# Kernel tuning notes

Hardware: AMD Instinct MI355X
Metric: run time of the kernel (lower is better)

Reference implementation:

```python
import jax, jax.numpy as jnp
import numpy as np
import math

B, T, H, D = 4, 2048, 16, 64
C = H * D            # d_model = 1024
FF = 4096            # mlp_hidden_dim
N_LAYERS = 12
EPS = 1e-5


def setup_inputs() -> dict:
    key = jax.random.key(0)
    ks = jax.random.split(key, 8)
    res_scale = 1.0 / math.sqrt(2 * N_LAYERS)
    std_c = math.sqrt(2.0 / C)
    std_ff = math.sqrt(2.0 / FF)
    return {
        "x": jax.random.normal(ks[0], (B, T, C), jnp.float32),
        "ln1_w": jnp.ones((C,), jnp.float32),
        "ln1_b": jnp.zeros((C,), jnp.float32),
        # weights stored [in, out] (transposed vs torch nn.Linear.weight)
        "w_qkv": jax.random.normal(ks[1], (C, 3 * C), jnp.float32) * std_c,
        "b_qkv": jnp.zeros((3 * C,), jnp.float32),
        "w_o": jax.random.normal(ks[2], (C, C), jnp.float32) * std_c * res_scale,
        "b_o": jnp.zeros((C,), jnp.float32),
        "ln2_w": jnp.ones((C,), jnp.float32),
        "ln2_b": jnp.zeros((C,), jnp.float32),
        "w_fc": jax.random.normal(ks[3], (C, FF), jnp.float32) * std_c,
        "b_fc": jnp.zeros((FF,), jnp.float32),
        "w_out": jax.random.normal(ks[4], (FF, C), jnp.float32) * std_ff * res_scale,
        "b_out": jnp.zeros((C,), jnp.float32),
    }


def _layer_norm(x, w, b):
    m = jnp.mean(x, axis=-1, keepdims=True)
    v = jnp.mean(jnp.square(x - m), axis=-1, keepdims=True)
    return (x - m) * jax.lax.rsqrt(v + EPS) * w + b


def reference(x, ln1_w, ln1_b, w_qkv, b_qkv, w_o, b_o, ln2_w, ln2_b, w_fc, b_fc, w_out, b_out):
    Bx, Tx, Cx = x.shape
    # attention
    qkv = _layer_norm(x, ln1_w, ln1_b) @ w_qkv + b_qkv          # [B,T,3C]
    q, k, v = jnp.split(qkv, 3, axis=-1)
    q = q.reshape(Bx, Tx, H, D)
    k = k.reshape(Bx, Tx, H, D)
    v = v.reshape(Bx, Tx, H, D)
    att = jnp.einsum("bqhd,bkhd->bhqk", q, k) / math.sqrt(D)    # [B,H,T,T]
    mask = jnp.tril(jnp.ones((Tx, Tx), dtype=bool))
    att = jnp.where(mask, att, -jnp.inf)
    att = jax.nn.softmax(att, axis=-1)
    y = jnp.einsum("bhqk,bkhd->bqhd", att, v).reshape(Bx, Tx, Cx)
    x = x + y @ w_o + b_o
    # mlp (torch F.gelu default = exact erf gelu)
    h = jax.nn.gelu(_layer_norm(x, ln2_w, ln2_b) @ w_fc + b_fc, approximate=False)
    x = x + h @ w_out + b_out
    return x
```

## Files before the change

### kernel.cpp

```cpp
#include <hip/hip_runtime.h>
#include <hip/hip_bf16.h>
#include <cstdint>


#define B_ 4
#define T_ 2048
#define H_ 16
#define D_ 64
#define C_ 1024
#define FF_ 4096
#define M_ (B_ * T_)
#define QKV_N (3 * C_)

typedef __bf16 bf16x8 __attribute__((ext_vector_type(8)));
typedef __bf16 bf16x4 __attribute__((ext_vector_type(4)));
typedef float floatx4 __attribute__((ext_vector_type(4)));

#define MFMA16(a, b, c) __builtin_amdgcn_mfma_f32_16x16x32_bf16(a, b, c, 0, 0, 0)

__device__ __forceinline__ void gload16(const void* g, void* l) {
  __builtin_amdgcn_global_load_lds(
      (const __attribute__((address_space(1))) void*)g,
      (__attribute__((address_space(3))) void*)l, 16, 0, 0);
}

__device__ __forceinline__ void lds_fence() {
  asm volatile("s_waitcnt lgkmcnt(0)" ::: "memory");
}

__device__ __forceinline__ float gelu_f(float x) {
  const float k1 = 2.3021178518f;
  const float ck = 0.1029410426f;
  const float y = x * __builtin_fmaf(x * x, ck, k1);
  const float t = __builtin_amdgcn_exp2f(y);
  return x - x * __builtin_amdgcn_rcpf(t + 1.0f);
}

__global__ __launch_bounds__(256) void convert_transpose(
    const float* __restrict__ w, __bf16* __restrict__ wt, int K, int N) {
  __shared__ float tile[32][33];
  const int n0 = blockIdx.x * 32, k0 = blockIdx.y * 32;
  const int tx = threadIdx.x & 31, ty = threadIdx.x >> 5;
#pragma unroll
  for (int i = 0; i < 4; ++i)
    tile[ty + i * 8][tx] = w[(size_t)(k0 + ty + i * 8) * N + n0 + tx];
  __syncthreads();
#pragma unroll
  for (int i = 0; i < 4; ++i)
    wt[(size_t)(n0 + ty + i * 8) * K + k0 + tx] = (__bf16)tile[tx][ty + i * 8];
}

__global__ __launch_bounds__(256) void ln_kernel(
    const float* __restrict__ x, const float* __restrict__ w,
    const float* __restrict__ b, __bf16* __restrict__ out) {
  __shared__ float red[4];
  const int row = blockIdx.x, tid = threadIdx.x;
  const float4 v = ((const float4*)(x + (size_t)row * C_))[tid];
  float s = v.x + v.y + v.z + v.w;
#pragma unroll
  for (int off = 1; off < 64; off <<= 1) s += __shfl_xor(s, off, 64);
  if ((tid & 63) == 0) red[tid >> 6] = s;
  __syncthreads();
  const float mean = (red[0] + red[1] + red[2] + red[3]) * (1.0f / C_);
  __syncthreads();
  const float dx = v.x - mean, dy = v.y - mean, dz = v.z - mean, dw = v.w - mean;
  float s2 = dx * dx + dy * dy + dz * dz + dw * dw;
#pragma unroll
  for (int off = 1; off < 64; off <<= 1) s2 += __shfl_xor(s2, off, 64);
  if ((tid & 63) == 0) red[tid >> 6] = s2;
  __syncthreads();
  const float var = (red[0] + red[1] + red[2] + red[3]) * (1.0f / C_);
  const float rstd = rsqrtf(var + 1e-5f);
  const float4 wv = ((const float4*)w)[tid];
  const float4 bv = ((const float4*)b)[tid];
  bf16x4 o;
  o[0] = (__bf16)(dx * rstd * wv.x + bv.x);
  o[1] = (__bf16)(dy * rstd * wv.y + bv.y);
  o[2] = (__bf16)(dz * rstd * wv.z + bv.z);
  o[3] = (__bf16)(dw * rstd * wv.w + bv.w);
  *(bf16x4*)(out + (size_t)row * C_ + tid * 4) = o;
}

__device__ __forceinline__ void swizzle_mn(int gx, int gy, int* bm, int* bn) {
  const int linear = blockIdx.y * gx + blockIdx.x;
  const int xcd = linear & 7, idx = linear >> 3;
  const int band = gy >> 3;
  const int per_grp = band * 8;
  const int g = idx / per_grp, rem = idx % per_grp;
  *bm = xcd * band + rem % band;
  *bn = g * 8 + rem / band;
}

template <bool GELU, bool RESID, bool OUTBF16>
__global__ __launch_bounds__(256, 2) void gemm_kernel(
    const __bf16* __restrict__ A, const __bf16* __restrict__ BT,
    const float* __restrict__ bias, const float* __restrict__ resid,
    float* __restrict__ outF, __bf16* __restrict__ outB, int M, int N, int K) {
  __shared__ __bf16 As[128 * 64];
  __shared__ __bf16 Bs[128 * 64];
  const int tid = threadIdx.x;
  const int wave = tid >> 6, lane = tid & 63;
  const int lane15 = lane & 15, quad = lane >> 4;
  const int r7 = lane15 & 7;

  int bm, bn;
  swizzle_mn(gridDim.x, gridDim.y, &bm, &bn);
  const int m0 = bm * 128, n0 = bn * 128;
  const int wm = (wave >> 1) * 64, wn = (wave & 1) * 64;

  const int srow = lane >> 3;
  const int gc8 = (lane & 7) ^ srow;

  floatx4 acc[4][4] = {};

  for (int k0 = 0; k0 < K; k0 += 64) {
#pragma unroll
    for (int t = 0; t < 4; ++t) {
      const int row = wave * 32 + t * 8;
      gload16(A + (size_t)(m0 + row + srow) * K + k0 + gc8 * 8, &As[row * 64]);
      gload16(BT + (size_t)(n0 + row + srow) * K + k0 + gc8 * 8, &Bs[row * 64]);
    }
    __syncthreads();
#pragma unroll
    for (int kk8 = 0; kk8 < 8; kk8 += 4) {
      bf16x8 af[4], bfr[4];
#pragma unroll
      for (int i = 0; i < 4; ++i) {
        af[i] = *(const bf16x8*)
            &As[(wm + i * 16 + lane15) * 64 + (((kk8 + quad) ^ r7) << 3)];
        bfr[i] = *(const bf16x8*)
            &Bs[(wn + i * 16 + lane15) * 64 + (((kk8 + quad) ^ r7) << 3)];
      }
#pragma unroll
      for (int i = 0; i < 4; ++i)
#pragma unroll
        for (int j = 0; j < 4; ++j) acc[i][j] = MFMA16(af[i], bfr[j], acc[i][j]);
    }
    __syncthreads();
  }

#pragma unroll
  for (int mi = 0; mi < 4; ++mi) {
    const int row = m0 + wm + mi * 16 + quad * 4;
#pragma unroll
    for (int ni = 0; ni < 4; ++ni) {
      const int col = n0 + wn + ni * 16 + lane15;
      const float bsum = bias[col];
#pragma unroll
      for (int r = 0; r < 4; ++r) {
        const size_t idx2 = (size_t)(row + r) * N + col;
        float v = acc[mi][ni][r] + bsum;
        if (GELU) v = gelu_f(v);
        if (RESID) v += resid[idx2];
        if (OUTBF16) outB[idx2] = (__bf16)v;
        else outF[idx2] = v;
      }
    }
  }
}

template <bool GELU, bool RESID, bool OUTBF16>
__global__ __launch_bounds__(256, 4) void gemm_n64_kernel(
    const __bf16* __restrict__ A, const __bf16* __restrict__ BT,
    const float* __restrict__ bias, const float* __restrict__ resid,
    float* __restrict__ outF, __bf16* __restrict__ outB, int M, int N, int K) {
  __shared__ __bf16 As[128 * 64];
  __shared__ __bf16 Bs[64 * 64];
  const int tid = threadIdx.x;
  const int wave = tid >> 6, lane = tid & 63;
  const int lane15 = lane & 15, quad = lane >> 4;
  const int r7 = lane15 & 7;

  int bm, bn;
  swizzle_mn(gridDim.x, gridDim.y, &bm, &bn);
  const int m0 = bm * 128, n0 = bn * 64;
  const int wm = (wave >> 1) * 64, wn = (wave & 1) * 32;

  const int srow = lane >> 3;
  const int gc8 = (lane & 7) ^ srow;

  floatx4 acc[4][2] = {};

  for (int k0 = 0; k0 < K; k0 += 64) {
#pragma unroll
    for (int t = 0; t < 4; ++t) {
      const int row = wave * 32 + t * 8;
      gload16(A + (size_t)(m0 + row + srow) * K + k0 + gc8 * 8, &As[row * 64]);
    }
#pragma unroll
    for (int t = 0; t < 2; ++t) {
      const int row = wave * 16 + t * 8;
      gload16(BT + (size_t)(n0 + row + srow) * K + k0 + gc8 * 8, &Bs[row * 64]);
    }
    __syncthreads();
#pragma unroll
    for (int kk8 = 0; kk8 < 8; kk8 += 4) {
      bf16x8 af[4], bfr[2];
#pragma unroll
      for (int i = 0; i < 4; ++i)
        af[i] = *(const bf16x8*)
            &As[(wm + i * 16 + lane15) * 64 + (((kk8 + quad) ^ r7) << 3)];
#pragma unroll
      for (int j = 0; j < 2; ++j)
        bfr[j] = *(const bf16x8*)
            &Bs[(wn + j * 16 + lane15) * 64 + (((kk8 + quad) ^ r7) << 3)];
#pragma unroll
      for (int i = 0; i < 4; ++i)
#pragma unroll
        for (int j = 0; j < 2; ++j) acc[i][j] = MFMA16(af[i], bfr[j], acc[i][j]);
    }
    __syncthreads();
  }

#pragma unroll
  for (int mi = 0; mi < 4; ++mi) {
    const int row = m0 + wm + mi * 16 + quad * 4;
#pragma unroll
    for (int ni = 0; ni < 2; ++ni) {
      const int col = n0 + wn + ni * 16 + lane15;
      const float bsum = bias[col];
#pragma unroll
      for (int r = 0; r < 4; ++r) {
        const size_t idx2 = (size_t)(row + r) * N + col;
        float v = acc[mi][ni][r] + bsum;
        if (GELU) v = gelu_f(v);
        if (RESID) v += resid[idx2];
        if (OUTBF16) outB[idx2] = (__bf16)v;
        else outF[idx2] = v;
      }
    }
  }
}

#define PT_S 72
#define VT_S 72
__global__ __launch_bounds__(256, 4) void attn_kernel(
    const __bf16* __restrict__ qkv, __bf16* __restrict__ y) {
  const int linear = blockIdx.x;
  const int xcd = linear & 7, idx = linear >> 3;
  const int pair = idx & 15;
  const int bh = xcd * 8 + (idx >> 4);
  const int b = bh >> 4, h = bh & 15;

  const int tid = threadIdx.x, wave = tid >> 6, lane = tid & 63;
  const int lane15 = lane & 15, quad = lane >> 4;
  __shared__ __bf16 K0[2][64 * 32];
  __shared__ __bf16 K1[2][64 * 32];
  __shared__ __bf16 Vt[64 * VT_S];
  __shared__ __bf16 Pt[4][16 * PT_S];

  const int krow_loc = lane >> 2;
  const int kdc = (lane & 3) * 8;
  const int v_kvp = tid & 31;
  const int v_dgrp = tid >> 5;
  const float QSCALE = 0.125f * 1.44269504088896f;

  const int qt_of[2] = {pair, 31 - pair};

  bf16x8 onesf;
#pragma unroll
  for (int j = 0; j < 8; ++j) onesf[j] = (__bf16)1.0f;

  bf16x8 vr0, vr1;
  int g = 0;

  {
    const size_t gk =
        (size_t)(b * T_ + wave * 16 + krow_loc) * QKV_N + C_ + h * 64 + kdc;
    gload16(qkv + gk, &K0[0][wave * 16 * 32]);
    gload16(qkv + gk + 32, &K1[0][wave * 16 * 32]);
    const __bf16* vsrc = qkv + (size_t)(b * T_ + 2 * v_kvp) * QKV_N +
                         2 * C_ + h * 64 + v_dgrp * 8;
    vr0 = *(const bf16x8*)vsrc;
    vr1 = *(const bf16x8*)(vsrc + QKV_N);
  }

#pragma unroll
  for (int seg = 0; seg < 2; ++seg) {
    const int qt = qt_of[seg];
    const int qrow0 = qt * 64 + wave * 16;
    const int tq = qrow0 + lane15;

    bf16x8 qf0, qf1;
    {
      const size_t base =
          (size_t)(b * T_ + qrow0 + lane15) * QKV_N + h * 64 + quad * 8;
      const bf16x8 r0 = *(const bf16x8*)(qkv + base);
      const bf16x8 r1 = *(const bf16x8*)(qkv + base + 32);
#pragma unroll
      for (int j = 0; j < 8; ++j) {
        qf0[j] = (__bf16)((float)r0[j] * QSCALE);
        qf1[j] = (__bf16)((float)r1[j] * QSCALE);
      }
    }

    floatx4 o[4] = {};
    floatx4 o4 = {0.f, 0.f, 0.f, 0.f};

    const int ntiles = qt + 1;
    for (int kvt = 0; kvt < ntiles; ++kvt) {
      const int buf = g & 1;
      const int c0 = kvt * 64;
      __syncthreads();
#pragma unroll
      for (int j = 0; j < 8; ++j) {
        union { __bf16 hh[2]; uint32_t u; } pk;
        pk.hh[0] = vr0[j];
        pk.hh[1] = vr1[j];
        *(uint32_t*)&Vt[(v_dgrp * 8 + j) * VT_S + 2 * v_kvp] = pk.u;
      }
      __syncthreads();

      if (!(seg == 1 && kvt + 1 >= ntiles)) {
        const int nkvt = (kvt + 1 >= ntiles) ? 0 : kvt + 1;
        const int nc0 = nkvt * 64;
        const int nbuf = (g + 1) & 1;
        const size_t gk = (size_t)(b * T_ + nc0 + wave * 16 + krow_loc) * QKV_N +
                          C_ + h * 64 + kdc;
        gload16(qkv + gk, &K0[nbuf][wave * 16 * 32]);
        gload16(qkv + gk + 32, &K1[nbuf][wave * 16 * 32]);
        const __bf16* vsrc = qkv + (size_t)(b * T_ + nc0 + 2 * v_kvp) * QKV_N +
                             2 * C_ + h * 64 + v_dgrp * 8;
        vr0 = *(const bf16x8*)vsrc;
        vr1 = *(const bf16x8*)(vsrc + QKV_N);
      }

#pragma unroll
      for (int nt = 0; nt < 4; ++nt) {
        const bf16x8 kf0 =
            *(const bf16x8*)&K0[buf][(nt * 16 + lane15) * 32 + quad * 8];
        const bf16x8 kf1 =
            *(const bf16x8*)&K1[buf][(nt * 16 + lane15) * 32 + quad * 8];
        floatx4 s = {0.f, 0.f, 0.f, 0.f};
        s = MFMA16(kf0, qf0, s);
        s = MFMA16(kf1, qf1, s);
        const int tk0 = c0 + nt * 16 + quad * 4;
        bf16x4 pk4;
        if (kvt == qt) {
#pragma unroll
          for (int r = 0; r < 4; ++r) {
            const float sv = (tk0 + r <= tq) ? s[r] : -1e30f;
            pk4[r] = (__bf16)__builtin_amdgcn_exp2f(sv);
          }
        } else {
#pragma unroll
          for (int r = 0; r < 4; ++r)
            pk4[r] = (__bf16)__builtin_amdgcn_exp2f(s[r]);
        }
        *(bf16x4*)&Pt[wave][lane15 * PT_S + nt * 16 + quad * 4] = pk4;
      }
      lds_fence();

#pragma unroll
      for (int half = 0; half < 2; ++half) {
        const bf16x8 pf =
            *(const bf16x8*)&Pt[wave][lane15 * PT_S + half * 32 + quad * 8];
#pragma unroll
        for (int dt = 0; dt < 4; ++dt) {
          const bf16x8 vf =
              *(const bf16x8*)&Vt[(dt * 16 + lane15) * VT_S + half * 32 + quad * 8];
          o[dt] = MFMA16(pf, vf, o[dt]);
        }
        o4 = MFMA16(pf, onesf, o4);
      }
      ++g;
    }

#pragma unroll
    for (int r = 0; r < 4; ++r) {
      const int tqo = qrow0 + quad * 4 + r;
      const float inv = 1.0f / o4[r];
#pragma unroll
      for (int dt = 0; dt < 4; ++dt)
        y[(size_t)(b * T_ + tqo) * C_ + h * 64 + dt * 16 + lane15] =
            (__bf16)(o[dt][r] * inv);
    }
  }
}

extern "C" void kernel_launch(void* const* d_in, const int* in_sizes, int n_in,
                              void* d_out, int out_size, void* d_ws,
                              size_t ws_size, hipStream_t stream) {
  const float* x     = (const float*)d_in[0];
  const float* ln1_w = (const float*)d_in[1];
  const float* ln1_b = (const float*)d_in[2];
  const float* w_qkv = (const float*)d_in[3];
  const float* b_qkv = (const float*)d_in[4];
  const float* w_o   = (const float*)d_in[5];
  const float* b_o   = (const float*)d_in[6];
  const float* ln2_w = (const float*)d_in[7];
  const float* ln2_b = (const float*)d_in[8];
  const float* w_fc  = (const float*)d_in[9];
  const float* b_fc  = (const float*)d_in[10];
  const float* w_out = (const float*)d_in[11];
  const float* b_out = (const float*)d_in[12];

  char* ws = (char*)d_ws;
  __bf16* wqkvT = (__bf16*)(ws + 0);
  __bf16* woT   = (__bf16*)(ws + 6291456);
  __bf16* wfcT  = (__bf16*)(ws + 8388608);
  __bf16* woutT = (__bf16*)(ws + 16777216);
  __bf16* xn    = (__bf16*)(ws + 25165824);
  __bf16* qkv   = (__bf16*)(ws + 41943040);
  __bf16* yb    = (__bf16*)(ws + 92274688);
  float*  x1    = (float*)(ws + 109051904);
  __bf16* hb    = (__bf16*)(ws + 142606336);

  convert_transpose<<<dim3(QKV_N / 32, C_ / 32), 256, 0, stream>>>(w_qkv, wqkvT, C_, QKV_N);
  convert_transpose<<<dim3(C_ / 32, C_ / 32), 256, 0, stream>>>(w_o, woT, C_, C_);
  convert_transpose<<<dim3(FF_ / 32, C_ / 32), 256, 0, stream>>>(w_fc, wfcT, C_, FF_);
  convert_transpose<<<dim3(C_ / 32, FF_ / 32), 256, 0, stream>>>(w_out, woutT, FF_, C_);

  ln_kernel<<<M_, 256, 0, stream>>>(x, ln1_w, ln1_b, xn);
  gemm_kernel<false, false, true><<<dim3(QKV_N / 128, M_ / 128), 256, 0, stream>>>(
      xn, wqkvT, b_qkv, nullptr, nullptr, qkv, M_, QKV_N, C_);
  attn_kernel<<<1024, 256, 0, stream>>>(qkv, yb);
  gemm_n64_kernel<false, true, false><<<dim3(C_ / 64, M_ / 128), 256, 0, stream>>>(
      yb, woT, b_o, x, x1, nullptr, M_, C_, C_);
  ln_kernel<<<M_, 256, 0, stream>>>(x1, ln2_w, ln2_b, xn);
  gemm_kernel<true, false, true><<<dim3(FF_ / 128, M_ / 128), 256, 0, stream>>>(
      xn, wfcT, b_fc, nullptr, nullptr, hb, M_, FF_, C_);
  gemm_n64_kernel<false, true, false><<<dim3(C_ / 64, M_ / 128), 256, 0, stream>>>(
      hb, woutT, b_out, x1, (float*)d_out, nullptr, M_, C_, FF_);
}
```

Measured before the change: 475.0 us.

## Merge weight conversions, use lighter attention barriers, use 128-wide tile for MLP down-proj

Merges the four weight convert-transpose launches into a single kernel that dispatches on block index, saving launch overhead. In the attention loop, __syncthreads is replaced by raw s_barrier plus an explicit LDS waitcnt, so the barrier no longer waits on outstanding global loads. The final FF->C projection switches from the N=64 GEMM to the 128x128 GEMM, which halves the block count (512 blocks) in exchange for more reuse per block.

New measurement: 433.5 us. 1.1x faster.

```diff
diff --git a/kernel.cpp b/kernel.cpp
--- a/kernel.cpp
+++ b/kernel.cpp
@@ -28,6 +28,12 @@
   asm volatile("s_waitcnt lgkmcnt(0)" ::: "memory");
 }
 
+__device__ __forceinline__ void bar() {
+  asm volatile("" ::: "memory");
+  __builtin_amdgcn_s_barrier();
+  asm volatile("" ::: "memory");
+}
+
 __device__ __forceinline__ float gelu_f(float x) {
   const float k1 = 2.3021178518f;
   const float ck = 0.1029410426f;
@@ -36,18 +42,30 @@
   return x - x * __builtin_amdgcn_rcpf(t + 1.0f);
 }
 
-__global__ __launch_bounds__(256) void convert_transpose(
-    const float* __restrict__ w, __bf16* __restrict__ wt, int K, int N) {
+__global__ __launch_bounds__(256) void ct4_kernel(
+    const float* __restrict__ wqkv, const float* __restrict__ wo,
+    const float* __restrict__ wfc, const float* __restrict__ wout,
+    __bf16* __restrict__ dqkv, __bf16* __restrict__ dwo,
+    __bf16* __restrict__ dfc, __bf16* __restrict__ dwout) {
   __shared__ float tile[32][33];
-  const int n0 = blockIdx.x * 32, k0 = blockIdx.y * 32;
+  int bx = blockIdx.x;
+  const float* src;
+  __bf16* dst;
+  int K, N;
+  if (bx < 3072)      { src = wqkv; dst = dqkv; K = 1024; N = 3072; }
+  else if (bx < 4096) { bx -= 3072; src = wo;   dst = dwo;   K = 1024; N = 1024; }
+  else if (bx < 8192) { bx -= 4096; src = wfc;  dst = dfc;   K = 1024; N = 4096; }
+  else                { bx -= 8192; src = wout; dst = dwout; K = 4096; N = 1024; }
+  const int tn = N >> 5;
+  const int n0 = (bx % tn) * 32, k0 = (bx / tn) * 32;
   const int tx = threadIdx.x & 31, ty = threadIdx.x >> 5;
 #pragma unroll
   for (int i = 0; i < 4; ++i)
-    tile[ty + i * 8][tx] = w[(size_t)(k0 + ty + i * 8) * N + n0 + tx];
+    tile[ty + i * 8][tx] = src[(size_t)(k0 + ty + i * 8) * N + n0 + tx];
   __syncthreads();
 #pragma unroll
   for (int i = 0; i < 4; ++i)
-    wt[(size_t)(n0 + ty + i * 8) * K + k0 + tx] = (__bf16)tile[tx][ty + i * 8];
+    dst[(size_t)(n0 + ty + i * 8) * K + k0 + tx] = (__bf16)tile[tx][ty + i * 8];
 }
 
 __global__ __launch_bounds__(256) void ln_kernel(
@@ -301,7 +319,7 @@
     for (int kvt = 0; kvt < ntiles; ++kvt) {
       const int buf = g & 1;
       const int c0 = kvt * 64;
-      __syncthreads();
+      bar();
 #pragma unroll
       for (int j = 0; j < 8; ++j) {
         union { __bf16 hh[2]; uint32_t u; } pk;
@@ -309,7 +327,8 @@
         pk.hh[1] = vr1[j];
         *(uint32_t*)&Vt[(v_dgrp * 8 + j) * VT_S + 2 * v_kvp] = pk.u;
       }
-      __syncthreads();
+      lds_fence();
+      bar();
 
       if (!(seg == 1 && kvt + 1 >= ntiles)) {
         const int nkvt = (kvt + 1 >= ntiles) ? 0 : kvt + 1;
@@ -406,10 +425,8 @@
   float*  x1    = (float*)(ws + 109051904);
   __bf16* hb    = (__bf16*)(ws + 142606336);
 
-  convert_transpose<<<dim3(QKV_N / 32, C_ / 32), 256, 0, stream>>>(w_qkv, wqkvT, C_, QKV_N);
-  convert_transpose<<<dim3(C_ / 32, C_ / 32), 256, 0, stream>>>(w_o, woT, C_, C_);
-  convert_transpose<<<dim3(FF_ / 32, C_ / 32), 256, 0, stream>>>(w_fc, wfcT, C_, FF_);
-  convert_transpose<<<dim3(C_ / 32, FF_ / 32), 256, 0, stream>>>(w_out, woutT, FF_, C_);
+  ct4_kernel<<<12288, 256, 0, stream>>>(w_qkv, w_o, w_fc, w_out,
+                                        wqkvT, woT, wfcT, woutT);
 
   ln_kernel<<<M_, 256, 0, stream>>>(x, ln1_w, ln1_b, xn);
   gemm_kernel<false, false, true><<<dim3(QKV_N / 128, M_ / 128), 256, 0, stream>>>(
@@ -420,6 +437,6 @@
   ln_kernel<<<M_, 256, 0, stream>>>(x1, ln2_w, ln2_b, xn);
   gemm_kernel<true, false, true><<<dim3(FF_ / 128, M_ / 128), 256, 0, stream>>>(
       xn, wfcT, b_fc, nullptr, nullptr, hb, M_, FF_, C_);
-  gemm_n64_kernel<false, true, false><<<dim3(C_ / 64, M_ / 128), 256, 0, stream>>>(
+  gemm_kernel<false, true, false><<<dim3(C_ / 128, M_ / 128), 256, 0, stream>>>(
       hb, woutT, b_out, x1, (float*)d_out, nullptr, M_, C_, FF_);
 }
```
